# Kernel optimization log

Measured on AMD Instinct MI355X. Metric: run time of the kernel, lower is better.

## Reference

```python
import jax, jax.numpy as jnp
import numpy as np

TEMP = 0.07  # temperature used as logits / 0.07 in the original


def setup_inputs() -> dict:
    key = jax.random.key(0)
    k1, k2, k3 = jax.random.split(key, 3)
    B, N, T, L, D = 8, 128, 8, 6, 256
    meta = jax.random.normal(k1, (B, N, T, L, D), dtype=jnp.float32)
    thing = jax.random.randint(k2, (B, N, T), 0, 2, dtype=jnp.int32)
    label = jax.random.randint(k3, (B, N, T), 0, 40, dtype=jnp.int32)
    return {"meta_weight_for_con": meta, "thing_gt_idx": thing, "label_tmp": label}


def _con_loss(meta, thing, label):
    # meta: [B,N,T,L,D]; thing,label: [B,N,T]
    B, N, T, L, D = meta.shape
    P = N * T
    valid = thing.reshape(B, P).astype(bool)            # [B,P] boolean gt mask
    lab = label.reshape(B, P)                           # [B,P]
    # meta_weight_b[mask] -> [K,L,D]; permute(1,0,2) -> per-layer [K,D].
    # We keep all P positions and mask instead of compacting (jit-friendly).
    w = meta.reshape(B, P, L, D).transpose(0, 2, 1, 3)  # [B,L,P,D]
    w = w / jnp.maximum(jnp.linalg.norm(w, axis=-1, keepdims=True), 1e-12)  # F.normalize
    z = jnp.einsum('blpd,blqd->blpq', w, w) / TEMP      # similarity / temp [B,L,P,P]

    same = lab[:, :, None] == lab[:, None, :]           # [B,P,P]
    vpair = valid[:, :, None] & valid[:, None, :]
    eye = jnp.eye(P, dtype=bool)
    pos_mask = same & (~eye) & vpair                    # positives: same label, not self
    neg_mask = (~same) & vpair                          # negatives: different label

    K = valid.sum(axis=1)                               # [B] ins_num_ per batch
    pos_count = pos_mask.sum(axis=-1)                   # [B,P]
    neg_count = neg_mask.sum(axis=-1)                   # [B,P]

    # --- random positive sample per (batch, layer, row), mirroring np.random.choice ---
    u = jax.random.uniform(jax.random.key(42), (B, L, P))
    r = jnp.floor(u * pos_count[:, None, :].astype(u.dtype)).astype(jnp.int32)
    r = jnp.minimum(r, jnp.maximum(pos_count - 1, 0)[:, None, :])
    ranks = jnp.cumsum(pos_mask, axis=-1) - 1           # rank of each positive in index order
    sel = pos_mask[:, None, :, :] & (ranks[:, None, :, :] == r[..., None])  # [B,L,P,P]
    zp = jnp.sum(jnp.where(sel, z, 0.0), axis=-1)       # chosen positive logit [B,L,P]
    diag = jnp.diagonal(z, axis1=-2, axis2=-1)          # self-sim fallback when no positives
    zp = jnp.where((pos_count > 0)[:, None, :], zp, diag)

    # --- last negative (original pads by repeating the last negative to K-1) ---
    iota = jnp.arange(P)
    idx_last = jnp.max(jnp.where(neg_mask, iota[None, None, :], -1), axis=-1)  # [B,P]
    idx = jnp.broadcast_to(jnp.maximum(idx_last, 0)[:, None, :, None], (B, L, P, 1))
    zl = jnp.take_along_axis(z, idx, axis=-1)[..., 0]   # [B,L,P]

    # --- stable CE with label 0: loss = lse(logits) - zp ---
    max_n = jnp.max(jnp.where(neg_mask[:, None], z, -jnp.inf), axis=-1)  # [B,L,P]
    m = jnp.maximum(zp, max_n)
    m = jnp.where(jnp.isfinite(m), m, zp)
    sum_neg = jnp.sum(jnp.where(neg_mask[:, None], jnp.exp(z - m[..., None]), 0.0), axis=-1)
    pad = jnp.maximum((K[:, None] - 1 - neg_count), 0).astype(z.dtype)   # [B,P]
    pad_term = pad[:, None, :] * jnp.where((neg_count > 0)[:, None, :], jnp.exp(zl - m), 0.0)
    loss_row = m + jnp.log(jnp.exp(zp - m) + sum_neg + pad_term) - zp    # [B,L,P]

    row_w = valid.astype(z.dtype)
    mean_per = jnp.sum(loss_row * row_w[:, None, :], axis=-1) / jnp.maximum(K, 1)[:, None].astype(z.dtype)  # [B,L]

    gate = jnp.sum((thing.sum(axis=2) > 0), axis=1) >= 2  # skip batches with <2 gt rows
    return jnp.sum(jnp.where(gate[:, None], mean_per, 0.0))


def reference(meta_weight_for_con, thing_gt_idx, label_tmp):
    return _con_loss(meta_weight_for_con, thing_gt_idx, label_tmp)
```

## Files before the change

### kernel.cpp

```cpp
#include <hip/hip_runtime.h>
#include <stdint.h>

namespace {

constexpr int Bb = 8, Ll = 6, Dd = 256, Pp = 1024;
constexpr float SCALE_Y = 14.285714285714286f * 1.4426950408889634f;
constexpr float M0y = 21.0f;
constexpr float LN2f = 0.6931471805599453f;

typedef __attribute__((ext_vector_type(4))) float floatx4;

__device__ const int PAIRS[36] = {
  0x00,0x01,0x02,0x03,0x04,0x05,0x06,0x07,
  0x11,0x12,0x13,0x14,0x15,0x16,0x17,
  0x22,0x23,0x24,0x25,0x26,0x27,
  0x33,0x34,0x35,0x36,0x37,
  0x44,0x45,0x46,0x47,
  0x55,0x56,0x57,
  0x66,0x67,
  0x77
};

__device__ __forceinline__ void async16(const void* g, void* l) {
  __builtin_amdgcn_global_load_lds(
      (const __attribute__((address_space(1))) void*)g,
      (__attribute__((address_space(3))) void*)l, 16, 0, 0);
}

__device__ __forceinline__ uint32_t rotl32(uint32_t x, int n) {
  return (x << n) | (x >> (32 - n));
}
__device__ __forceinline__ void tf_round(uint32_t& x0, uint32_t& x1, int r) {
  x0 += x1; x1 = rotl32(x1, r); x1 ^= x0;
}
__device__ void threefry2x32(uint32_t x0, uint32_t x1, uint32_t& o0, uint32_t& o1) {
  const uint32_t k0 = 0u, k1 = 42u;
  const uint32_t k2 = k0 ^ k1 ^ 0x1BD11BDAu;
  x0 += k0; x1 += k1;
  tf_round(x0,x1,13); tf_round(x0,x1,15); tf_round(x0,x1,26); tf_round(x0,x1,6);
  x0 += k1; x1 += k2 + 1u;
  tf_round(x0,x1,17); tf_round(x0,x1,29); tf_round(x0,x1,16); tf_round(x0,x1,24);
  x0 += k2; x1 += k0 + 2u;
  tf_round(x0,x1,13); tf_round(x0,x1,15); tf_round(x0,x1,26); tf_round(x0,x1,6);
  x0 += k0; x1 += k1 + 3u;
  tf_round(x0,x1,17); tf_round(x0,x1,29); tf_round(x0,x1,16); tf_round(x0,x1,24);
  x0 += k1; x1 += k2 + 4u;
  tf_round(x0,x1,13); tf_round(x0,x1,15); tf_round(x0,x1,26); tf_round(x0,x1,6);
  x0 += k2; x1 += k0 + 5u;
  o0 = x0; o1 = x1;
}
__device__ float jax_u01(uint32_t idx) {
  const uint32_t HALF = (uint32_t)(Bb * Ll * Pp / 2);
  uint32_t o0, o1, bits;
  if (idx < HALF) { threefry2x32(idx, idx + HALF, o0, o1); bits = o0; }
  else            { threefry2x32(idx - HALF, idx, o0, o1); bits = o1; }
  return __uint_as_float((bits >> 9) | 0x3f800000u) - 1.0f;
}

__device__ __forceinline__ uint32_t fp8e4m3_rne(float x) {
  uint32_t u = __float_as_uint(x);
  const uint32_t s = (u >> 24) & 0x80u;
  u &= 0x7FFFFFFFu;
  uint32_t code;
  if (u < 0x3C800000u) {
    code = (uint32_t)__float2int_rn(__uint_as_float(u) * 512.0f);
  } else {
    const uint32_t r = (u + 0x7FFFFu + ((u >> 20) & 1u)) >> 20;
    code = r - (120u << 3);
  }
  return s | code;
}
__device__ __forceinline__ float fp8e4m3_tof(uint32_t c) {
  const uint32_t e = (c >> 3) & 15u, m = c & 7u;
  float mag;
  if (e) mag = __uint_as_float(((e + 120u) << 23) | (m << 20));
  else   mag = (float)m * 0.001953125f;
  return (c & 0x80u) ? -mag : mag;
}

__device__ __forceinline__ void fp8x4_tof(uint32_t u, float f[4]) {
#if __has_builtin(__builtin_amdgcn_cvt_f32_fp8)
  f[0] = __builtin_amdgcn_cvt_f32_fp8((int)u, 0);
  f[1] = __builtin_amdgcn_cvt_f32_fp8((int)u, 1);
  f[2] = __builtin_amdgcn_cvt_f32_fp8((int)u, 2);
  f[3] = __builtin_amdgcn_cvt_f32_fp8((int)u, 3);
#else
  f[0] = fp8e4m3_tof(u & 0xFF);
  f[1] = fp8e4m3_tof((u >> 8) & 0xFF);
  f[2] = fp8e4m3_tof((u >> 16) & 0xFF);
  f[3] = fp8e4m3_tof((u >> 24) & 0xFF);
#endif
}

constexpr int NB_NORM = Bb * Pp * Ll / 4;
constexpr int NB_ROW  = Bb * Pp / 4;

__global__ void prep_k(const float* __restrict__ meta, const int* __restrict__ thing,
                       const int* __restrict__ label, uint8_t* __restrict__ wn,
                       int* __restrict__ qpos, int* __restrict__ negc,
                       int* __restrict__ qidx, int* __restrict__ Kv,
                       int* __restrict__ gatev, float* __restrict__ rowsum_g,
                       float* __restrict__ out) {
  __shared__ int sK[256], sG[256];
  const int bid = blockIdx.x, t = threadIdx.x;

  if (bid < NB_NORM) {
    const int wid = (bid * 256 + t) >> 6;
    const int lane = t & 63;
    const float4 v = *(const float4*)(meta + (size_t)wid * Dd + lane * 4);
    float ss = v.x * v.x + v.y * v.y + v.z * v.z + v.w * v.w;
    #pragma unroll
    for (int m = 32; m; m >>= 1) ss += __shfl_xor(ss, m, 64);
    const float inv = 1.0f / fmaxf(sqrtf(ss), 1e-12f);
    const int bp = wid / Ll, l = wid - bp * Ll;
    const int b = bp >> 10, p = bp & (Pp - 1);
    uint8_t* dst = wn + ((size_t)(b * Ll + l) * Pp + p) * Dd + lane * 4;
#if __has_builtin(__builtin_amdgcn_cvt_pk_fp8_f32)
    const int lo16 = __builtin_amdgcn_cvt_pk_fp8_f32(v.x * inv, v.y * inv, 0, false);
    const uint32_t packed =
        (uint32_t)__builtin_amdgcn_cvt_pk_fp8_f32(v.z * inv, v.w * inv, lo16, true);
#else
    const uint32_t packed = fp8e4m3_rne(v.x * inv)
                          | (fp8e4m3_rne(v.y * inv) << 8)
                          | (fp8e4m3_rne(v.z * inv) << 16)
                          | (fp8e4m3_rne(v.w * inv) << 24);
#endif
    *(uint32_t*)dst = packed;
    return;
  }
  if (bid < NB_NORM + NB_ROW) {
    const int wid = (bid - NB_NORM) * 4 + (t >> 6);
    const int lane = t & 63;
    const int b = wid >> 10, p = wid & (Pp - 1);
    const int* lab = label + b * Pp;
    const int* th  = thing + b * Pp;
    const int myLab = lab[p];
    const bool myValid = (th[p] != 0);

    uint32_t posbits = 0;
    int cnt[16];
    int pc = 0, nc = 0, last = -1;
    #pragma unroll
    for (int c = 0; c < 16; ++c) {
      const int q = c * 64 + lane;
      const int lq = lab[q];
      const bool vq = (th[q] != 0);
      const bool same = (lq == myLab);
      const bool pos = myValid && vq && same && (q != p);
      const bool neg = myValid && vq && !same;
      uint64_t bp2 = __ballot(pos);
      uint64_t bn = __ballot(neg);
      if (pos) posbits |= (1u << c);
      cnt[c] = __popcll(bp2);
      pc += cnt[c];
      nc += __popcll(bn);
      if (bn) last = c * 64 + 63 - __clzll(bn);
    }
    int qsel[Ll];
    #pragma unroll
    for (int l = 0; l < Ll; ++l) qsel[l] = p;
    if (pc > 0) {
      for (int l = 0; l < Ll; ++l) {
        const float u = jax_u01((uint32_t)((b * Ll + l) * Pp + p));
        int r = (int)floorf(u * (float)pc);
        r = min(r, pc - 1);
        int base = 0;
        for (int c = 0; c < 16; ++c) {
          if (r < base + cnt[c]) {
            const bool mine = (posbits >> c) & 1u;
            uint64_t bm = __ballot(mine);
            uint64_t ltmask = (lane == 0) ? 0ull : (~0ull >> (64 - lane));
            int myrank = __popcll(bm & ltmask);
            bool hit = mine && (base + myrank == r);
            uint64_t hb = __ballot(hit);
            qsel[l] = c * 64 + (int)__builtin_ctzll(hb);
            break;
          }
          base += cnt[c];
        }
      }
    }
    if (lane == 0) {
      negc[wid] = nc;
      qidx[wid] = (last < 0) ? 0 : last;
      #pragma unroll
      for (int l = 0; l < Ll; ++l) qpos[(b * Ll + l) * Pp + p] = qsel[l];
    }
    return;
  }
  if (bid < NB_NORM + NB_ROW + Bb) {
    const int b = bid - (NB_NORM + NB_ROW);
    int k = 0;
    for (int p = t; p < Pp; p += 256) k += (thing[b * Pp + p] != 0);
    int g = 0;
    if (t < 128) {
      int any = 0;
      for (int tt = 0; tt < 8; ++tt) any |= (thing[(b * 128 + t) * 8 + tt] != 0);
      g = any;
    }
    sK[t] = k; sG[t] = g;
    __syncthreads();
    for (int s = 128; s; s >>= 1) {
      if (t < s) { sK[t] += sK[t + s]; sG[t] += sG[t + s]; }
      __syncthreads();
    }
    if (t == 0) { Kv[b] = sK[0]; gatev[b] = (sG[0] >= 2) ? 1 : 0; }
    return;
  }
  if (bid < NB_NORM + NB_ROW + Bb + 48) {
    const int idx = (bid - (NB_NORM + NB_ROW + Bb)) * 256 + t;
    *(float4*)(rowsum_g + idx * 4) = (float4){0.f, 0.f, 0.f, 0.f};
    return;
  }
  if (t == 0) out[0] = 0.f;
}

__global__ __launch_bounds__(256)
void gemm_loss_k(const uint8_t* __restrict__ wn,
                 const int* __restrict__ thing, const int* __restrict__ label,
                 float* __restrict__ rowsum_g) {
  __shared__ __align__(16) uint8_t As[2 * 128 * 64];
  __shared__ __align__(16) uint8_t Bs[2 * 128 * 64];
  __shared__ int labp_s[128], valp_s[128], labq_s[128], valq_s[128];
  __shared__ float rowsum_lds[128], colsum_lds[128];

  const int t = threadIdx.x;
  const int bid = blockIdx.x;
  const int xcd = bid & 7;
  const int chunk = bid >> 3;
  const int bl = xcd + 8 * (chunk % 6);
  const int b = bl / Ll;
  const int pair = PAIRS[chunk / 6];
  const int pt = pair >> 4, qt = pair & 15;
  const bool diag = (pt == qt);
  const int p0 = pt * 128, q0 = qt * 128;

  if (t < 128) {
    labp_s[t] = label[b * Pp + p0 + t];
    valp_s[t] = thing[b * Pp + p0 + t];
    labq_s[t] = label[b * Pp + q0 + t];
    valq_s[t] = thing[b * Pp + q0 + t];
    rowsum_lds[t] = 0.f;
    colsum_lds[t] = 0.f;
  }

  const uint8_t* Wbl = wn + (size_t)bl * Pp * Dd;
  const int lane = t & 63;
  const int w = t >> 6, wr = w >> 1, wc = w & 1;
  const int cq = lane & 15, rq = lane >> 4;
  const int wbase16 = (t & ~63) * 16;

  floatx4 acc[4][4];
  #pragma unroll
  for (int i = 0; i < 4; ++i)
    #pragma unroll
    for (int j = 0; j < 4; ++j) acc[i][j] = (floatx4){0.f, 0.f, 0.f, 0.f};

  auto STAGE = [&](int bsel, int kt) {
    const int k0 = kt * 64;
    #pragma unroll
    for (int rd = 0; rd < 2; ++rd) {
      const int c = rd * 256 + t;
      const int row = c >> 2, sp2 = c & 3;
      const int sl = sp2 ^ ((row >> 1) & 3);
      async16(Wbl + (size_t)(p0 + row) * Dd + k0 + sl * 16,
              As + bsel * 8192 + rd * 4096 + wbase16);
      if (!diag)
        async16(Wbl + (size_t)(q0 + row) * Dd + k0 + sl * 16,
                Bs + bsel * 8192 + rd * 4096 + wbase16);
    }
  };

  STAGE(0, 0);
  __syncthreads();

  for (int kt = 0; kt < 4; ++kt) {
    const int bsel = kt & 1;
    if (kt < 3) STAGE(bsel ^ 1, kt + 1);
    const uint8_t* Ab = As + bsel * 8192;
    const uint8_t* Bb2 = diag ? Ab : (Bs + bsel * 8192);
    #pragma unroll
    for (int sub = 0; sub < 2; ++sub) {
      const int Lw = sub * 2 + (rq >> 1);
      const int off8 = (rq & 1) * 8;
      long long af[4], bfr[4];
      #pragma unroll
      for (int fi = 0; fi < 4; ++fi) {
        const int row = wr * 64 + fi * 16 + cq;
        af[fi] = *(const long long*)(Ab + row * 64 + (Lw ^ ((row >> 1) & 3)) * 16 + off8);
      }
      #pragma unroll
      for (int fj = 0; fj < 4; ++fj) {
        const int row = wc * 64 + fj * 16 + cq;
        bfr[fj] = *(const long long*)(Bb2 + row * 64 + (Lw ^ ((row >> 1) & 3)) * 16 + off8);
      }
      #pragma unroll
      for (int fi = 0; fi < 4; ++fi)
        #pragma unroll
        for (int fj = 0; fj < 4; ++fj)
          acc[fi][fj] = __builtin_amdgcn_mfma_f32_16x16x32_fp8_fp8(af[fi], bfr[fj],
                                                                   acc[fi][fj], 0, 0, 0);
    }
    __syncthreads();
  }

  int qlabv[4];
  float qvalf[4];
  float csum[4] = {0.f, 0.f, 0.f, 0.f};
  #pragma unroll
  for (int fj = 0; fj < 4; ++fj) {
    const int cl = wc * 64 + fj * 16 + cq;
    qlabv[fj] = labq_s[cl];
    qvalf[fj] = valq_s[cl] ? 1.f : 0.f;
  }
  #pragma unroll
  for (int fi = 0; fi < 4; ++fi) {
    #pragma unroll
    for (int reg = 0; reg < 4; ++reg) {
      const int rl = wr * 64 + fi * 16 + rq * 4 + reg;
      const int rlab = labp_s[rl];
      const float rvalf = valp_s[rl] ? 1.f : 0.f;
      float rsum = 0.f;
      #pragma unroll
      for (int fj = 0; fj < 4; ++fj) {
        const float y = acc[fi][fj][reg] * SCALE_Y;
        const float negm = (qlabv[fj] != rlab) ? (qvalf[fj] * rvalf) : 0.f;
        const float term = negm * exp2f(y - M0y);
        rsum += term;
        csum[fj] += term;
      }
      rsum += __shfl_xor(rsum, 1); rsum += __shfl_xor(rsum, 2);
      rsum += __shfl_xor(rsum, 4); rsum += __shfl_xor(rsum, 8);
      if (cq == 0) atomicAdd(&rowsum_lds[rl], rsum);
    }
  }
  if (!diag) {
    #pragma unroll
    for (int fj = 0; fj < 4; ++fj) {
      float c = csum[fj];
      c += __shfl_xor(c, 16); c += __shfl_xor(c, 32);
      if (rq == 0) atomicAdd(&colsum_lds[wc * 64 + fj * 16 + cq], c);
    }
  }
  __syncthreads();
  if (t < 128) {
    atomicAdd(&rowsum_g[bl * Pp + p0 + t], rowsum_lds[t]);
    if (!diag) atomicAdd(&rowsum_g[bl * Pp + q0 + t], colsum_lds[t]);
  }
}

__global__ void final_k(const uint8_t* __restrict__ wn,
                        const int* __restrict__ qpos, const int* __restrict__ qidx,
                        const float* __restrict__ rowsum_g, const int* __restrict__ negc,
                        const int* __restrict__ thing, const int* __restrict__ Kv,
                        const int* __restrict__ gatev, float* __restrict__ out) {
  const int t = threadIdx.x, lane = t & 63, wv = t >> 6;
  const int bl = blockIdx.x >> 5;
  const int b = bl / Ll;
  const int p0 = (blockIdx.x & 31) * 32 + wv * 8;
  float acc = 0.f;
  if (gatev[b]) {
    const int Kb = Kv[b];
    const float invK = 1.f / (float)max(Kb, 1);
    const uint8_t* W = wn + (size_t)bl * Pp * Dd;
    for (int i = 0; i < 8; ++i) {
      const int p = p0 + i;
      if (thing[b * Pp + p] == 0) continue;
      const int qp = qpos[bl * Pp + p];
      const int qi = qidx[b * Pp + p];
      const uint32_t a4 = *(const uint32_t*)(W + (size_t)p  * Dd + lane * 4);
      const uint32_t b4 = *(const uint32_t*)(W + (size_t)qp * Dd + lane * 4);
      const uint32_t c4 = *(const uint32_t*)(W + (size_t)qi * Dd + lane * 4);
      float fa[4], fb[4], fc[4];
      fp8x4_tof(a4, fa);
      fp8x4_tof(b4, fb);
      fp8x4_tof(c4, fc);
      float sp = 0.f, sl = 0.f;
      #pragma unroll
      for (int j = 0; j < 4; ++j) {
        sp += fa[j] * fb[j];
        sl += fa[j] * fc[j];
      }
      #pragma unroll
      for (int m = 32; m; m >>= 1) {
        sp += __shfl_xor(sp, m, 64);
        sl += __shfl_xor(sl, m, 64);
      }
      if (lane == 0) {
        const float yp = sp * SCALE_Y, yl = sl * SCALE_Y;
        const float rs = rowsum_g[bl * Pp + p];
        const int nc = negc[b * Pp + p];
        const float pad = fmaxf((float)(Kb - 1 - nc), 0.f);
        const float tot = exp2f(yp - M0y) + rs + ((nc > 0) ? pad * exp2f(yl - M0y) : 0.f);
        acc += LN2f * (M0y + log2f(tot) - yp) * invK;
      }
    }
  }
  __shared__ float sb[256];
  sb[t] = acc;
  __syncthreads();
  for (int s = 128; s; s >>= 1) {
    if (t < s) sb[t] += sb[t + s];
    __syncthreads();
  }
  if (t == 0 && sb[0] != 0.f) atomicAdd(out, sb[0]);
}

}

extern "C" void kernel_launch(void* const* d_in, const int* in_sizes, int n_in,
                              void* d_out, int out_size, void* d_ws, size_t ws_size,
                              hipStream_t stream) {
  const float* meta = (const float*)d_in[0];
  const int* thing  = (const int*)d_in[1];
  const int* label  = (const int*)d_in[2];
  float* out = (float*)d_out;

  char* ws = (char*)d_ws;
  size_t off = 0;
  uint8_t* wn = (uint8_t*)(ws + off); off += (size_t)Bb * Ll * Pp * Dd;
  int* qpos  = (int*)(ws + off); off += (size_t)Bb * Ll * Pp * 4;
  int* negc  = (int*)(ws + off); off += (size_t)Bb * Pp * 4;
  int* qidx  = (int*)(ws + off); off += (size_t)Bb * Pp * 4;
  int* Kv    = (int*)(ws + off); off += 64;
  int* gatev = (int*)(ws + off); off += 64;
  float* rowsum_g = (float*)(ws + off); off += (size_t)Bb * Ll * Pp * 4;

  const int nb_prep = NB_NORM + NB_ROW + Bb + 48 + 1;
  prep_k<<<nb_prep, 256, 0, stream>>>(meta, thing, label, wn, qpos, negc, qidx,
                                      Kv, gatev, rowsum_g, out);
  gemm_loss_k<<<1728, 256, 0, stream>>>(wn, thing, label, rowsum_g);
  final_k<<<1536, 256, 0, stream>>>(wn, qpos, qidx, rowsum_g, negc, thing, Kv, gatev, out);
}
```

Baseline: 163.2 us.

## Fuse prep, GEMM-loss and final kernels into one persistent kernel with grid barriers

Merges the three launches into one persistent kernel with a fixed grid of 512 blocks. The grid-stride loops cover normalisation, row stats, the fp8 MFMA similarity tiles and the final loss, with software grid barriers between phases. A tiny init kernel resets the barrier counters and the output. This removes inter-kernel launch gaps and tail effects, but adds spin-wait barrier cost and relies on all 512 blocks being co-resident. It may also lose the occupancy that 1728 independent GEMM blocks had.

```diff
diff --git a/kernel.cpp b/kernel.cpp
--- a/kernel.cpp
+++ b/kernel.cpp
@@ -4,6 +4,7 @@
 namespace {
 
 constexpr int Bb = 8, Ll = 6, Dd = 256, Pp = 1024;
+constexpr int GRID = 512;
 constexpr float SCALE_Y = 14.285714285714286f * 1.4426950408889634f;
 constexpr float M0y = 21.0f;
 constexpr float LN2f = 0.6931471805599453f;
@@ -25,6 +26,18 @@
   __builtin_amdgcn_global_load_lds(
       (const __attribute__((address_space(1))) void*)g,
       (__attribute__((address_space(3))) void*)l, 16, 0, 0);
+}
+
+__device__ __forceinline__ void grid_barrier(int* bar, int target) {
+  __syncthreads();
+  __threadfence();
+  if (threadIdx.x == 0) {
+    __hip_atomic_fetch_add(bar, 1, __ATOMIC_RELEASE, __HIP_MEMORY_SCOPE_AGENT);
+    while (__hip_atomic_load(bar, __ATOMIC_ACQUIRE, __HIP_MEMORY_SCOPE_AGENT) < target)
+      __builtin_amdgcn_s_sleep(4);
+  }
+  __syncthreads();
+  __threadfence();
 }
 
 __device__ __forceinline__ uint32_t rotl32(uint32_t x, int n) {
@@ -94,19 +107,33 @@
 
 constexpr int NB_NORM = Bb * Pp * Ll / 4;
 constexpr int NB_ROW  = Bb * Pp / 4;
-
-__global__ void prep_k(const float* __restrict__ meta, const int* __restrict__ thing,
-                       const int* __restrict__ label, uint8_t* __restrict__ wn,
-                       int* __restrict__ qpos, int* __restrict__ negc,
-                       int* __restrict__ qidx, int* __restrict__ Kv,
-                       int* __restrict__ gatev, float* __restrict__ rowsum_g,
-                       float* __restrict__ out) {
+constexpr int NT_GEMM = 8 * 6 * 36;
+constexpr int NB_FIN  = Bb * Ll * 32;
+
+__global__ void init_k(int* __restrict__ bar, float* __restrict__ out) {
+  if (threadIdx.x < 2) bar[threadIdx.x] = 0;
+  if (threadIdx.x == 0) out[0] = 0.f;
+}
+
+__global__ __launch_bounds__(256, 2)
+void fused_k(const float* __restrict__ meta, const int* __restrict__ thing,
+             const int* __restrict__ label, uint8_t* __restrict__ wn,
+             int* __restrict__ qpos, int* __restrict__ negc,
+             int* __restrict__ qidx, int* __restrict__ Kv,
+             int* __restrict__ gatev, float* __restrict__ rowsum_g,
+             int* __restrict__ bar, float* __restrict__ out) {
+  __shared__ __align__(16) uint8_t As[2 * 128 * 64];
+  __shared__ __align__(16) uint8_t Bs[2 * 128 * 64];
+  __shared__ int labp_s[128], valp_s[128], labq_s[128], valq_s[128];
+  __shared__ float rowsum_lds[128], colsum_lds[128];
   __shared__ int sK[256], sG[256];
-  const int bid = blockIdx.x, t = threadIdx.x;
-
-  if (bid < NB_NORM) {
-    const int wid = (bid * 256 + t) >> 6;
-    const int lane = t & 63;
+  __shared__ float sb[256];
+
+  const int t = threadIdx.x, bid = blockIdx.x;
+  const int lane = t & 63;
+
+  for (int u = bid; u < NB_NORM; u += GRID) {
+    const int wid = u * 4 + (t >> 6);
     const float4 v = *(const float4*)(meta + (size_t)wid * Dd + lane * 4);
     float ss = v.x * v.x + v.y * v.y + v.z * v.z + v.w * v.w;
     #pragma unroll
@@ -126,11 +153,10 @@
                           | (fp8e4m3_rne(v.w * inv) << 24);
 #endif
     *(uint32_t*)dst = packed;
-    return;
-  }
-  if (bid < NB_NORM + NB_ROW) {
-    const int wid = (bid - NB_NORM) * 4 + (t >> 6);
-    const int lane = t & 63;
+  }
+
+  for (int u = bid; u < NB_ROW; u += GRID) {
+    const int wid = u * 4 + (t >> 6);
     const int b = wid >> 10, p = wid & (Pp - 1);
     const int* lab = label + b * Pp;
     const int* th  = thing + b * Pp;
@@ -161,8 +187,8 @@
     for (int l = 0; l < Ll; ++l) qsel[l] = p;
     if (pc > 0) {
       for (int l = 0; l < Ll; ++l) {
-        const float u = jax_u01((uint32_t)((b * Ll + l) * Pp + p));
-        int r = (int)floorf(u * (float)pc);
+        const float uu = jax_u01((uint32_t)((b * Ll + l) * Pp + p));
+        int r = (int)floorf(uu * (float)pc);
         r = min(r, pc - 1);
         int base = 0;
         for (int c = 0; c < 16; ++c) {
@@ -186,10 +212,10 @@
       #pragma unroll
       for (int l = 0; l < Ll; ++l) qpos[(b * Ll + l) * Pp + p] = qsel[l];
     }
-    return;
-  }
-  if (bid < NB_NORM + NB_ROW + Bb) {
-    const int b = bid - (NB_NORM + NB_ROW);
+  }
+
+  if (bid < Bb) {
+    const int b = bid;
     int k = 0;
     for (int p = t; p < Pp; p += 256) k += (thing[b * Pp + p] != 0);
     int g = 0;
@@ -205,161 +231,150 @@
       __syncthreads();
     }
     if (t == 0) { Kv[b] = sK[0]; gatev[b] = (sG[0] >= 2) ? 1 : 0; }
-    return;
-  }
-  if (bid < NB_NORM + NB_ROW + Bb + 48) {
-    const int idx = (bid - (NB_NORM + NB_ROW + Bb)) * 256 + t;
+  }
+
+  if (bid < 48) {
+    const int idx = bid * 256 + t;
     *(float4*)(rowsum_g + idx * 4) = (float4){0.f, 0.f, 0.f, 0.f};
-    return;
-  }
-  if (t == 0) out[0] = 0.f;
-}
-
-__global__ __launch_bounds__(256)
-void gemm_loss_k(const uint8_t* __restrict__ wn,
-                 const int* __restrict__ thing, const int* __restrict__ label,
-                 float* __restrict__ rowsum_g) {
-  __shared__ __align__(16) uint8_t As[2 * 128 * 64];
-  __shared__ __align__(16) uint8_t Bs[2 * 128 * 64];
-  __shared__ int labp_s[128], valp_s[128], labq_s[128], valq_s[128];
-  __shared__ float rowsum_lds[128], colsum_lds[128];
-
-  const int t = threadIdx.x;
-  const int bid = blockIdx.x;
-  const int xcd = bid & 7;
-  const int chunk = bid >> 3;
-  const int bl = xcd + 8 * (chunk % 6);
-  const int b = bl / Ll;
-  const int pair = PAIRS[chunk / 6];
-  const int pt = pair >> 4, qt = pair & 15;
-  const bool diag = (pt == qt);
-  const int p0 = pt * 128, q0 = qt * 128;
-
-  if (t < 128) {
-    labp_s[t] = label[b * Pp + p0 + t];
-    valp_s[t] = thing[b * Pp + p0 + t];
-    labq_s[t] = label[b * Pp + q0 + t];
-    valq_s[t] = thing[b * Pp + q0 + t];
-    rowsum_lds[t] = 0.f;
-    colsum_lds[t] = 0.f;
-  }
-
-  const uint8_t* Wbl = wn + (size_t)bl * Pp * Dd;
-  const int lane = t & 63;
+  }
+
+  grid_barrier(bar + 0, GRID);
+
   const int w = t >> 6, wr = w >> 1, wc = w & 1;
   const int cq = lane & 15, rq = lane >> 4;
   const int wbase16 = (t & ~63) * 16;
 
-  floatx4 acc[4][4];
-  #pragma unroll
-  for (int i = 0; i < 4; ++i)
-    #pragma unroll
-    for (int j = 0; j < 4; ++j) acc[i][j] = (floatx4){0.f, 0.f, 0.f, 0.f};
-
-  auto STAGE = [&](int bsel, int kt) {
-    const int k0 = kt * 64;
-    #pragma unroll
-    for (int rd = 0; rd < 2; ++rd) {
-      const int c = rd * 256 + t;
-      const int row = c >> 2, sp2 = c & 3;
-      const int sl = sp2 ^ ((row >> 1) & 3);
-      async16(Wbl + (size_t)(p0 + row) * Dd + k0 + sl * 16,
-              As + bsel * 8192 + rd * 4096 + wbase16);
-      if (!diag)
-        async16(Wbl + (size_t)(q0 + row) * Dd + k0 + sl * 16,
-                Bs + bsel * 8192 + rd * 4096 + wbase16);
-    }
-  };
-
-  STAGE(0, 0);
-  __syncthreads();
-
-  for (int kt = 0; kt < 4; ++kt) {
-    const int bsel = kt & 1;
-    if (kt < 3) STAGE(bsel ^ 1, kt + 1);
-    const uint8_t* Ab = As + bsel * 8192;
-    const uint8_t* Bb2 = diag ? Ab : (Bs + bsel * 8192);
-    #pragma unroll
-    for (int sub = 0; sub < 2; ++sub) {
-      const int Lw = sub * 2 + (rq >> 1);
-      const int off8 = (rq & 1) * 8;
-      long long af[4], bfr[4];
-      #pragma unroll
-      for (int fi = 0; fi < 4; ++fi) {
-        const int row = wr * 64 + fi * 16 + cq;
-        af[fi] = *(const long long*)(Ab + row * 64 + (Lw ^ ((row >> 1) & 3)) * 16 + off8);
-      }
+  for (int tile = bid; tile < NT_GEMM; tile += GRID) {
+    const int xcd = tile & 7;
+    const int chunk = tile >> 3;
+    const int bl = xcd + 8 * (chunk % 6);
+    const int b = bl / Ll;
+    const int pair = PAIRS[chunk / 6];
+    const int pt = pair >> 4, qt = pair & 15;
+    const bool diag = (pt == qt);
+    const int p0 = pt * 128, q0 = qt * 128;
+
+    __syncthreads();
+    if (t < 128) {
+      labp_s[t] = label[b * Pp + p0 + t];
+      valp_s[t] = thing[b * Pp + p0 + t];
+      labq_s[t] = label[b * Pp + q0 + t];
+      valq_s[t] = thing[b * Pp + q0 + t];
+      rowsum_lds[t] = 0.f;
+      colsum_lds[t] = 0.f;
+    }
+
+    const uint8_t* Wbl = wn + (size_t)bl * Pp * Dd;
+
+    floatx4 acc[4][4];
+    #pragma unroll
+    for (int i = 0; i < 4; ++i)
+      #pragma unroll
+      for (int j = 0; j < 4; ++j) acc[i][j] = (floatx4){0.f, 0.f, 0.f, 0.f};
+
+    auto STAGE = [&](int bsel, int kt) {
+      const int k0 = kt * 64;
+      #pragma unroll
+      for (int rd = 0; rd < 2; ++rd) {
+        const int c = rd * 256 + t;
+        const int row = c >> 2, sp2 = c & 3;
+        const int sl = sp2 ^ ((row >> 1) & 3);
+        async16(Wbl + (size_t)(p0 + row) * Dd + k0 + sl * 16,
+                As + bsel * 8192 + rd * 4096 + wbase16);
+        if (!diag)
+          async16(Wbl + (size_t)(q0 + row) * Dd + k0 + sl * 16,
+                  Bs + bsel * 8192 + rd * 4096 + wbase16);
+      }
+    };
+
+    STAGE(0, 0);
+    __syncthreads();
+
+    const uint8_t* Bbase0 = diag ? As : Bs;
+    for (int kt = 0; kt < 4; ++kt) {
+      const int bsel = kt & 1;
+      if (kt < 3) STAGE(bsel ^ 1, kt + 1);
+      const uint8_t* Ab = As + bsel * 8192;
+      const uint8_t* Bb2 = Bbase0 + bsel * 8192;
+      #pragma unroll
+      for (int sub = 0; sub < 2; ++sub) {
+        const int Lw = sub * 2 + (rq >> 1);
+        const int off8 = (rq & 1) * 8;
+        long long af[4], bfr[4];
+        #pragma unroll
+        for (int fi = 0; fi < 4; ++fi) {
+          const int row = wr * 64 + fi * 16 + cq;
+          af[fi] = *(const long long*)(Ab + row * 64 + (Lw ^ ((row >> 1) & 3)) * 16 + off8);
+        }
+        #pragma unroll
+        for (int fj = 0; fj < 4; ++fj) {
+          const int row = wc * 64 + fj * 16 + cq;
+          bfr[fj] = *(const long long*)(Bb2 + row * 64 + (Lw ^ ((row >> 1) & 3)) * 16 + off8);
+        }
+        #pragma unroll
+        for (int fi = 0; fi < 4; ++fi)
+          #pragma unroll
+          for (int fj = 0; fj < 4; ++fj)
+            acc[fi][fj] = __builtin_amdgcn_mfma_f32_16x16x32_fp8_fp8(af[fi], bfr[fj],
+                                                                     acc[fi][fj], 0, 0, 0);
+      }
+      __syncthreads();
+    }
+
+    int qlabv[4];
+    float qvalf[4];
+    float csum[4] = {0.f, 0.f, 0.f, 0.f};
+    #pragma unroll
+    for (int fj = 0; fj < 4; ++fj) {
+      const int cl = wc * 64 + fj * 16 + cq;
+      qlabv[fj] = labq_s[cl];
+      qvalf[fj] = valq_s[cl] ? 1.f : 0.f;
+    }
+    #pragma unroll
+    for (int fi = 0; fi < 4; ++fi) {
+      #pragma unroll
+      for (int reg = 0; reg < 4; ++reg) {
+        const int rl = wr * 64 + fi * 16 + rq * 4 + reg;
+        const int rlab = labp_s[rl];
+        const float rvalf = valp_s[rl] ? 1.f : 0.f;
+        float rsum = 0.f;
+        #pragma unroll
+        for (int fj = 0; fj < 4; ++fj) {
+          const float y = acc[fi][fj][reg] * SCALE_Y;
+          const float negm = (qlabv[fj] != rlab) ? (qvalf[fj] * rvalf) : 0.f;
+          const float term = negm * exp2f(y - M0y);
+          rsum += term;
+          csum[fj] += term;
+        }
+        rsum += __shfl_xor(rsum, 1); rsum += __shfl_xor(rsum, 2);
+        rsum += __shfl_xor(rsum, 4); rsum += __shfl_xor(rsum, 8);
+        if (cq == 0) atomicAdd(&rowsum_lds[rl], rsum);
+      }
+    }
+    if (!diag) {
       #pragma unroll
       for (int fj = 0; fj < 4; ++fj) {
-        const int row = wc * 64 + fj * 16 + cq;
-        bfr[fj] = *(const long long*)(Bb2 + row * 64 + (Lw ^ ((row >> 1) & 3)) * 16 + off8);
-      }
-      #pragma unroll
-      for (int fi = 0; fi < 4; ++fi)
-        #pragma unroll
-        for (int fj = 0; fj < 4; ++fj)
-          acc[fi][fj] = __builtin_amdgcn_mfma_f32_16x16x32_fp8_fp8(af[fi], bfr[fj],
-                                                                   acc[fi][fj], 0, 0, 0);
+        float c = csum[fj];
+        c += __shfl_xor(c, 16); c += __shfl_xor(c, 32);
+        if (rq == 0) atomicAdd(&colsum_lds[wc * 64 + fj * 16 + cq], c);
+      }
     }
     __syncthreads();
-  }
-
-  int qlabv[4];
-  float qvalf[4];
-  float csum[4] = {0.f, 0.f, 0.f, 0.f};
-  #pragma unroll
-  for (int fj = 0; fj < 4; ++fj) {
-    const int cl = wc * 64 + fj * 16 + cq;
-    qlabv[fj] = labq_s[cl];
-    qvalf[fj] = valq_s[cl] ? 1.f : 0.f;
-  }
-  #pragma unroll
-  for (int fi = 0; fi < 4; ++fi) {
-    #pragma unroll
-    for (int reg = 0; reg < 4; ++reg) {
-      const int rl = wr * 64 + fi * 16 + rq * 4 + reg;
-      const int rlab = labp_s[rl];
-      const float rvalf = valp_s[rl] ? 1.f : 0.f;
-      float rsum = 0.f;
-      #pragma unroll
-      for (int fj = 0; fj < 4; ++fj) {
-        const float y = acc[fi][fj][reg] * SCALE_Y;
-        const float negm = (qlabv[fj] != rlab) ? (qvalf[fj] * rvalf) : 0.f;
-        const float term = negm * exp2f(y - M0y);
-        rsum += term;
-        csum[fj] += term;
-      }
-      rsum += __shfl_xor(rsum, 1); rsum += __shfl_xor(rsum, 2);
-      rsum += __shfl_xor(rsum, 4); rsum += __shfl_xor(rsum, 8);
-      if (cq == 0) atomicAdd(&rowsum_lds[rl], rsum);
-    }
-  }
-  if (!diag) {
-    #pragma unroll
-    for (int fj = 0; fj < 4; ++fj) {
-      float c = csum[fj];
-      c += __shfl_xor(c, 16); c += __shfl_xor(c, 32);
-      if (rq == 0) atomicAdd(&colsum_lds[wc * 64 + fj * 16 + cq], c);
-    }
-  }
-  __syncthreads();
-  if (t < 128) {
-    atomicAdd(&rowsum_g[bl * Pp + p0 + t], rowsum_lds[t]);
-    if (!diag) atomicAdd(&rowsum_g[bl * Pp + q0 + t], colsum_lds[t]);
-  }
-}
-
-__global__ void final_k(const uint8_t* __restrict__ wn,
-                        const int* __restrict__ qpos, const int* __restrict__ qidx,
-                        const float* __restrict__ rowsum_g, const int* __restrict__ negc,
-                        const int* __restrict__ thing, const int* __restrict__ Kv,
-                        const int* __restrict__ gatev, float* __restrict__ out) {
-  const int t = threadIdx.x, lane = t & 63, wv = t >> 6;
-  const int bl = blockIdx.x >> 5;
-  const int b = bl / Ll;
-  const int p0 = (blockIdx.x & 31) * 32 + wv * 8;
-  float acc = 0.f;
-  if (gatev[b]) {
+    if (t < 128) {
+      atomicAdd(&rowsum_g[bl * Pp + p0 + t], rowsum_lds[t]);
+      if (!diag) atomicAdd(&rowsum_g[bl * Pp + q0 + t], colsum_lds[t]);
+    }
+  }
+
+  grid_barrier(bar + 1, GRID);
+
+  float accl = 0.f;
+  const int wv = t >> 6;
+  for (int u = bid; u < NB_FIN; u += GRID) {
+    const int bl = u >> 5;
+    const int b = bl / Ll;
+    if (!gatev[b]) continue;
+    const int p0 = (u & 31) * 32 + wv * 8;
     const int Kb = Kv[b];
     const float invK = 1.f / (float)max(Kb, 1);
     const uint8_t* W = wn + (size_t)bl * Pp * Dd;
@@ -388,16 +403,17 @@
       }
       if (lane == 0) {
         const float yp = sp * SCALE_Y, yl = sl * SCALE_Y;
-        const float rs = rowsum_g[bl * Pp + p];
+        const float rs = __hip_atomic_load(&rowsum_g[bl * Pp + p],
+                                           __ATOMIC_RELAXED, __HIP_MEMORY_SCOPE_AGENT);
         const int nc = negc[b * Pp + p];
         const float pad = fmaxf((float)(Kb - 1 - nc), 0.f);
         const float tot = exp2f(yp - M0y) + rs + ((nc > 0) ? pad * exp2f(yl - M0y) : 0.f);
-        acc += LN2f * (M0y + log2f(tot) - yp) * invK;
-      }
-    }
-  }
-  __shared__ float sb[256];
-  sb[t] = acc;
+        accl += LN2f * (M0y + log2f(tot) - yp) * invK;
+      }
+    }
+  }
+  __syncthreads();
+  sb[t] = accl;
   __syncthreads();
   for (int s = 128; s; s >>= 1) {
     if (t < s) sb[t] += sb[t + s];
@@ -425,10 +441,9 @@
   int* Kv    = (int*)(ws + off); off += 64;
   int* gatev = (int*)(ws + off); off += 64;
   float* rowsum_g = (float*)(ws + off); off += (size_t)Bb * Ll * Pp * 4;
-
-  const int nb_prep = NB_NORM + NB_ROW + Bb + 48 + 1;
-  prep_k<<<nb_prep, 256, 0, stream>>>(meta, thing, label, wn, qpos, negc, qidx,
-                                      Kv, gatev, rowsum_g, out);
-  gemm_loss_k<<<1728, 256, 0, stream>>>(wn, thing, label, rowsum_g);
-  final_k<<<1536, 256, 0, stream>>>(wn, qpos, qidx, rowsum_g, negc, thing, Kv, gatev, out);
-}
+  int* bar   = (int*)(ws + off); off += 64;
+
+  init_k<<<1, 64, 0, stream>>>(bar, out);
+  fused_k<<<GRID, 256, 0, stream>>>(meta, thing, label, wn, qpos, negc, qidx,
+                                    Kv, gatev, rowsum_g, bar, out);
+}
```

After: 389.2 us. 2.38x slower.

## Fuse final loss pass into GEMM kernel via per-row-tile completion counters

Applied to the files above, without the earlier changes.

Merges the separate final_k launch into the GEMM kernel. Each tile block bumps an atomic counter for its row tiles, and the last block to finish a 128-row tile computes the per-row loss terms for that tile. This removes one kernel launch and its dependency gap, and the counters are zeroed in the prep kernel. In exchange it adds fences and atomics, the tail work now runs on a few blocks per tile, and the launch bounds hint changes to 4 waves.

```diff
diff --git a/kernel.cpp b/kernel.cpp
--- a/kernel.cpp
+++ b/kernel.cpp
@@ -100,7 +100,7 @@
                        int* __restrict__ qpos, int* __restrict__ negc,
                        int* __restrict__ qidx, int* __restrict__ Kv,
                        int* __restrict__ gatev, float* __restrict__ rowsum_g,
-                       float* __restrict__ out) {
+                       int* __restrict__ cnt2, float* __restrict__ out) {
   __shared__ int sK[256], sG[256];
   const int bid = blockIdx.x, t = threadIdx.x;
 
@@ -208,21 +208,28 @@
     return;
   }
   if (bid < NB_NORM + NB_ROW + Bb + 48) {
-    const int idx = (bid - (NB_NORM + NB_ROW + Bb)) * 256 + t;
+    const int zb = bid - (NB_NORM + NB_ROW + Bb);
+    const int idx = zb * 256 + t;
     *(float4*)(rowsum_g + idx * 4) = (float4){0.f, 0.f, 0.f, 0.f};
+    if (zb == 0 && t < 192) { cnt2[t] = 0; cnt2[t + 192] = 0; }
     return;
   }
   if (t == 0) out[0] = 0.f;
 }
 
-__global__ __launch_bounds__(256)
-void gemm_loss_k(const uint8_t* __restrict__ wn,
+__global__ __launch_bounds__(256, 4)
+void gemmfinal_k(const uint8_t* __restrict__ wn,
                  const int* __restrict__ thing, const int* __restrict__ label,
-                 float* __restrict__ rowsum_g) {
+                 const int* __restrict__ qpos, const int* __restrict__ qidx,
+                 const int* __restrict__ negc, const int* __restrict__ Kv,
+                 const int* __restrict__ gatev, float* __restrict__ rowsum_g,
+                 int* __restrict__ cnt2, float* __restrict__ out) {
   __shared__ __align__(16) uint8_t As[2 * 128 * 64];
   __shared__ __align__(16) uint8_t Bs[2 * 128 * 64];
   __shared__ int labp_s[128], valp_s[128], labq_s[128], valq_s[128];
   __shared__ float rowsum_lds[128], colsum_lds[128];
+  __shared__ int fin_s[2];
+  __shared__ float sb[256];
 
   const int t = threadIdx.x;
   const int bid = blockIdx.x;
@@ -274,11 +281,12 @@
   STAGE(0, 0);
   __syncthreads();
 
+  const uint8_t* Bbase0 = diag ? As : Bs;
   for (int kt = 0; kt < 4; ++kt) {
     const int bsel = kt & 1;
     if (kt < 3) STAGE(bsel ^ 1, kt + 1);
     const uint8_t* Ab = As + bsel * 8192;
-    const uint8_t* Bb2 = diag ? Ab : (Bs + bsel * 8192);
+    const uint8_t* Bb2 = Bbase0 + bsel * 8192;
     #pragma unroll
     for (int sub = 0; sub < 2; ++sub) {
       const int Lw = sub * 2 + (rq >> 1);
@@ -347,57 +355,68 @@
     atomicAdd(&rowsum_g[bl * Pp + p0 + t], rowsum_lds[t]);
     if (!diag) atomicAdd(&rowsum_g[bl * Pp + q0 + t], colsum_lds[t]);
   }
-}
-
-__global__ void final_k(const uint8_t* __restrict__ wn,
-                        const int* __restrict__ qpos, const int* __restrict__ qidx,
-                        const float* __restrict__ rowsum_g, const int* __restrict__ negc,
-                        const int* __restrict__ thing, const int* __restrict__ Kv,
-                        const int* __restrict__ gatev, float* __restrict__ out) {
-  const int t = threadIdx.x, lane = t & 63, wv = t >> 6;
-  const int bl = blockIdx.x >> 5;
-  const int b = bl / Ll;
-  const int p0 = (blockIdx.x & 31) * 32 + wv * 8;
-  float acc = 0.f;
-  if (gatev[b]) {
+  __syncthreads();
+
+  if (t == 0) {
+    __threadfence();
+    const int n1 = __hip_atomic_fetch_add(&cnt2[bl * 8 + pt], 1,
+                                          __ATOMIC_ACQ_REL, __HIP_MEMORY_SCOPE_AGENT);
+    fin_s[0] = (n1 == 7);
+    int f1 = 0;
+    if (!diag) {
+      const int n2 = __hip_atomic_fetch_add(&cnt2[bl * 8 + qt], 1,
+                                            __ATOMIC_ACQ_REL, __HIP_MEMORY_SCOPE_AGENT);
+      f1 = (n2 == 7);
+    }
+    fin_s[1] = f1;
+  }
+  __syncthreads();
+
+  float accl = 0.f;
+  if ((fin_s[0] | fin_s[1]) && gatev[b]) {
     const int Kb = Kv[b];
     const float invK = 1.f / (float)max(Kb, 1);
-    const uint8_t* W = wn + (size_t)bl * Pp * Dd;
-    for (int i = 0; i < 8; ++i) {
-      const int p = p0 + i;
-      if (thing[b * Pp + p] == 0) continue;
-      const int qp = qpos[bl * Pp + p];
-      const int qi = qidx[b * Pp + p];
-      const uint32_t a4 = *(const uint32_t*)(W + (size_t)p  * Dd + lane * 4);
-      const uint32_t b4 = *(const uint32_t*)(W + (size_t)qp * Dd + lane * 4);
-      const uint32_t c4 = *(const uint32_t*)(W + (size_t)qi * Dd + lane * 4);
-      float fa[4], fb[4], fc[4];
-      fp8x4_tof(a4, fa);
-      fp8x4_tof(b4, fb);
-      fp8x4_tof(c4, fc);
-      float sp = 0.f, sl = 0.f;
-      #pragma unroll
-      for (int j = 0; j < 4; ++j) {
-        sp += fa[j] * fb[j];
-        sl += fa[j] * fc[j];
+    #pragma unroll
+    for (int fr = 0; fr < 2; ++fr) {
+      if (!fin_s[fr]) continue;
+      const int pr = fr ? qt : pt;
+      const int rbase = pr * 128 + w * 32;
+      for (int i = 0; i < 32; ++i) {
+        const int p = rbase + i;
+        if (thing[b * Pp + p] == 0) continue;
+        const int qp = qpos[bl * Pp + p];
+        const int qi = qidx[b * Pp + p];
+        const uint32_t a4 = *(const uint32_t*)(Wbl + (size_t)p  * Dd + lane * 4);
+        const uint32_t b4 = *(const uint32_t*)(Wbl + (size_t)qp * Dd + lane * 4);
+        const uint32_t c4 = *(const uint32_t*)(Wbl + (size_t)qi * Dd + lane * 4);
+        float fa[4], fb[4], fc[4];
+        fp8x4_tof(a4, fa);
+        fp8x4_tof(b4, fb);
+        fp8x4_tof(c4, fc);
+        float sp = 0.f, sl = 0.f;
+        #pragma unroll
+        for (int j = 0; j < 4; ++j) {
+          sp += fa[j] * fb[j];
+          sl += fa[j] * fc[j];
+        }
+        #pragma unroll
+        for (int m = 32; m; m >>= 1) {
+          sp += __shfl_xor(sp, m, 64);
+          sl += __shfl_xor(sl, m, 64);
+        }
+        if (lane == 0) {
+          const float yp = sp * SCALE_Y, yl = sl * SCALE_Y;
+          const float rs = __hip_atomic_load(&rowsum_g[bl * Pp + p],
+                                             __ATOMIC_RELAXED, __HIP_MEMORY_SCOPE_AGENT);
+          const int nc = negc[b * Pp + p];
+          const float pad = fmaxf((float)(Kb - 1 - nc), 0.f);
+          const float tot = exp2f(yp - M0y) + rs + ((nc > 0) ? pad * exp2f(yl - M0y) : 0.f);
+          accl += LN2f * (M0y + log2f(tot) - yp) * invK;
+        }
       }
-      #pragma unroll
-      for (int m = 32; m; m >>= 1) {
-        sp += __shfl_xor(sp, m, 64);
-        sl += __shfl_xor(sl, m, 64);
-      }
-      if (lane == 0) {
-        const float yp = sp * SCALE_Y, yl = sl * SCALE_Y;
-        const float rs = rowsum_g[bl * Pp + p];
-        const int nc = negc[b * Pp + p];
-        const float pad = fmaxf((float)(Kb - 1 - nc), 0.f);
-        const float tot = exp2f(yp - M0y) + rs + ((nc > 0) ? pad * exp2f(yl - M0y) : 0.f);
-        acc += LN2f * (M0y + log2f(tot) - yp) * invK;
-      }
-    }
-  }
-  __shared__ float sb[256];
-  sb[t] = acc;
+    }
+  }
+  sb[t] = accl;
   __syncthreads();
   for (int s = 128; s; s >>= 1) {
     if (t < s) sb[t] += sb[t + s];
@@ -425,10 +444,11 @@
   int* Kv    = (int*)(ws + off); off += 64;
   int* gatev = (int*)(ws + off); off += 64;
   float* rowsum_g = (float*)(ws + off); off += (size_t)Bb * Ll * Pp * 4;
+  int* cnt2  = (int*)(ws + off); off += 384 * 4;
 
   const int nb_prep = NB_NORM + NB_ROW + Bb + 48 + 1;
   prep_k<<<nb_prep, 256, 0, stream>>>(meta, thing, label, wn, qpos, negc, qidx,
-                                      Kv, gatev, rowsum_g, out);
-  gemm_loss_k<<<1728, 256, 0, stream>>>(wn, thing, label, rowsum_g);
-  final_k<<<1536, 256, 0, stream>>>(wn, qpos, qidx, rowsum_g, negc, thing, Kv, gatev, out);
-}
+                                      Kv, gatev, rowsum_g, cnt2, out);
+  gemmfinal_k<<<8 * 6 * 36, 256, 0, stream>>>(wn, thing, label, qpos, qidx, negc,
+                                              Kv, gatev, rowsum_g, cnt2, out);
+}
```

Result: slower. 269.5 us (+65.2%).
